# Performance work log

Hardware: AMD Instinct MI355X
Metric: run time of the kernel (lower is better)

The kernel has to match this reference:

```python
import jax, jax.numpy as jnp
import numpy as np

D = 1024
H = 8
DK = D // H
BS, NSEG, NSEN = 16, 64, 32


def _linear_params(key, d_in, d_out, scale=0.02):
    kw, kb = jax.random.split(key)
    w = jax.random.normal(kw, (d_out, d_in), dtype=jnp.float32) * scale
    b = jax.random.normal(kb, (d_out,), dtype=jnp.float32) * scale
    return w, b


def setup_inputs() -> dict:
    key = jax.random.key(0)
    ks = jax.random.split(key, 12)
    A = jax.random.normal(ks[0], (BS, NSEG, D), dtype=jnp.float32)
    V = jax.random.normal(ks[1], (BS, NSEG, D), dtype=jnp.float32)
    S = jax.random.normal(ks[2], (BS, NSEN, D), dtype=jnp.float32)
    wA, bA = _linear_params(ks[3], D, D)
    wV, bV = _linear_params(ks[4], D, D)
    wS, bS = _linear_params(ks[5], D, D)
    wq, bq = _linear_params(ks[6], D, D)
    wk, bk = _linear_params(ks[7], D, D)
    wv, bv = _linear_params(ks[8], D, D)
    w1, b1 = _linear_params(ks[9], D, D)
    w2, b2 = _linear_params(ks[10], D, D)
    return {"A": A, "V": V, "S": S,
            "wA": wA, "bA": bA, "wV": wV, "bV": bV, "wS": wS, "bS": bS,
            "wq": wq, "bq": bq, "wk": wk, "bk": bk, "wv": wv, "bv": bv,
            "w1": w1, "b1": b1, "w2": w2, "b2": b2}


def _lin(x, w, b):
    return x @ w.T + b


def reference(A, V, S, wA, bA, wV, bV, wS, bS, wq, bq, wk, bk, wv, bv, w1, b1, w2, b2):
    bs, num_seg, d_model = A.shape
    num_sen = S.shape[1]
    A = _lin(A, wA, bA)
    V = _lin(V, wV, bV)
    S = _lin(S, wS, bS)
    av = jnp.stack([A, V], axis=2)                       # (bs, num_seg, 2, d)
    q = _lin(S, wq, bq).reshape(bs, num_sen, H, DK)      # (b, s, h, dk)
    k = _lin(av, wk, bk).reshape(bs, num_seg, 2, H, DK)  # (b, g, a, h, dk)
    v = _lin(av, wv, bv).reshape(bs, num_seg, 2, H, DK)
    # attention over the size-2 A/V axis only
    attn = jnp.einsum('bshd,bgahd->bsgah', q, k) / np.sqrt(DK).astype(np.float32)
    attn = jax.nn.softmax(attn, axis=3)                  # softmax over a (A vs V)
    out = jnp.einsum('bsgah,bgahd->bsghd', attn, v)
    out = out.reshape(bs, num_sen, num_seg, d_model)
    # positionwise FF: Linear -> ReLU -> Linear (dropout p=0)
    out = _lin(jax.nn.relu(_lin(out, w1, b1)), w2, b2)
    return out
```

## Files before the change

kernel.cpp:

```cpp
#include <hip/hip_runtime.h>
#include <stdint.h>


#define D_MODEL 1024
#define N_HEAD  8
#define DK      128
#define BS      16
#define NSEG    64
#define NSEN    32

typedef __attribute__((ext_vector_type(8))) __bf16 bf16x8;
typedef __attribute__((ext_vector_type(8))) unsigned short u16x8;
typedef __attribute__((ext_vector_type(4))) float f32x4;

__device__ __forceinline__ float bf2f(unsigned short b) {
  union { unsigned int u; float f; } x; x.u = ((unsigned int)b) << 16; return x.f;
}
__device__ __forceinline__ unsigned short f2bf(float f) {
  union { float f; unsigned int u; } x; x.f = f;
  unsigned int u = x.u;
  unsigned int r = (u + 0x7fffu + ((u >> 16) & 1u)) >> 16;
  return (unsigned short)r;
}

__device__ __forceinline__ void g2l16(const void* g, void* l) {
  __builtin_amdgcn_global_load_lds(
      (const __attribute__((address_space(1))) void*)g,
      (__attribute__((address_space(3))) void*)l, 16, 0, 0);
}

struct CvtB { const float* s[11]; unsigned short* d[11]; int n4[11]; };
__global__ __launch_bounds__(256)
void cvtall_kernel(CvtB p) {
  const int z = blockIdx.y;
  const int i = blockIdx.x * 256 + threadIdx.x;
  if (i >= p.n4[z]) return;
  float4 v = reinterpret_cast<const float4*>(p.s[z])[i];
  ushort4 o;
  o.x = f2bf(v.x); o.y = f2bf(v.y); o.z = f2bf(v.z); o.w = f2bf(v.w);
  reinterpret_cast<ushort4*>(p.d[z])[i] = o;
}

struct GSeg { const unsigned short* A; const unsigned short* B;
              const float* bias; unsigned short* C; };
struct GBatch { GSeg s[3]; int end[3]; };

__global__ __launch_bounds__(256, 3)
void gemm128_bt(GBatch gb) {
  __shared__ __align__(16) unsigned short lds[3 * 8192];

  const int nwg = gridDim.x;
  const int sw = (blockIdx.x & 7) * (nwg >> 3) + (blockIdx.x >> 3);
  int sgi = 0, base = 0;
  if (sw >= gb.end[0]) { sgi = 1; base = gb.end[0]; }
  if (sw >= gb.end[1]) { sgi = 2; base = gb.end[1]; }
  const GSeg sg = gb.s[sgi];
  const int st = sw - base;
  const int m0 = (st >> 3) * 128, n0 = (st & 7) * 128;

  const int T = threadIdx.x;
  const int lane = T & 63, wave = T >> 6;
  const int wr = wave >> 1, wc = wave & 1;
  const int fr = lane & 15, kg = lane >> 4;

  char* ldsc = (char*)lds;

  const int srow = T >> 2;
  const int gsl = ((T & 3) ^ ((srow & 3) ^ ((srow >> 2) & 3))) * 8;
  const unsigned short* A0 = sg.A + (size_t)(m0 + srow) * 1024 + gsl;
  const unsigned short* A1 = sg.A + (size_t)(m0 + 64 + srow) * 1024 + gsl;
  const unsigned short* B0 = sg.B + (size_t)(n0 + srow) * 1024 + gsl;
  const unsigned short* B1 = sg.B + (size_t)(n0 + 64 + srow) * 1024 + gsl;

  auto stage = [&](int buf, int k0) {
    char* d = ldsc + buf * 16384;
    g2l16(A0 + k0, d + T * 16);
    g2l16(A1 + k0, d + 4096 + T * 16);
    g2l16(B0 + k0, d + 8192 + T * 16);
    g2l16(B1 + k0, d + 12288 + T * 16);
  };

  int raddr[4], baddr[4];
#pragma unroll
  for (int mi = 0; mi < 4; ++mi) {
    int ra = wr * 64 + mi * 16 + fr;
    raddr[mi] = ra * 64 + ((kg ^ ((ra & 3) ^ ((ra >> 2) & 3))) * 16);
  }
#pragma unroll
  for (int ni = 0; ni < 4; ++ni) {
    int rb = wc * 64 + ni * 16 + fr;
    baddr[ni] = 8192 + rb * 64 + ((kg ^ ((rb & 3) ^ ((rb >> 2) & 3))) * 16);
  }

  f32x4 acc[4][4] = {};
  u16x8 f0[8], f1[8];

#define G128_LOAD(DST, BUF)                                                    \
  {                                                                            \
    const char* bp_ = ldsc + (BUF) * 16384;                                    \
    _Pragma("unroll")                                                          \
    for (int mi = 0; mi < 4; ++mi)                                             \
      DST[mi] = *reinterpret_cast<const u16x8*>(bp_ + raddr[mi]);              \
    _Pragma("unroll")                                                          \
    for (int ni = 0; ni < 4; ++ni)                                             \
      DST[4 + ni] = *reinterpret_cast<const u16x8*>(bp_ + baddr[ni]);          \
  }

#define G128_MFMA(SRC)                                                         \
  {                                                                            \
    __builtin_amdgcn_s_setprio(1);                                             \
    _Pragma("unroll")                                                          \
    for (int ni = 0; ni < 4; ++ni)                                             \
      _Pragma("unroll")                                                        \
      for (int mi = 0; mi < 4; ++mi)                                           \
        acc[ni][mi] = __builtin_amdgcn_mfma_f32_16x16x32_bf16(                 \
            __builtin_bit_cast(bf16x8, SRC[4 + ni]),                           \
            __builtin_bit_cast(bf16x8, SRC[mi]), acc[ni][mi], 0, 0, 0);        \
    __builtin_amdgcn_s_setprio(0);                                             \
  }

#define G128_ITER(T_, CUR, NXT)                                                \
  {                                                                            \
    if ((T_) + 2 < NT) stage(((T_) + 2) % 3, ((T_) + 2) * 32);                 \
    if ((T_) + 1 < NT) {                                                       \
      if ((T_) + 2 < NT) asm volatile("s_waitcnt vmcnt(4)" ::: "memory");      \
      else               asm volatile("s_waitcnt vmcnt(0)" ::: "memory");      \
      __builtin_amdgcn_s_barrier();                                            \
      G128_LOAD(NXT, ((T_) + 1) % 3);                                          \
    }                                                                          \
    G128_MFMA(CUR);                                                            \
  }

  const int NT = 32;
  stage(0, 0);
  stage(1, 32);
  asm volatile("s_waitcnt vmcnt(4)" ::: "memory");
  __builtin_amdgcn_s_barrier();
  G128_LOAD(f0, 0);

  for (int it = 0; it < NT; it += 2) {
    G128_ITER(it,     f0, f1);
    G128_ITER(it + 1, f1, f0);
  }

#pragma unroll
  for (int ni = 0; ni < 4; ++ni) {
    const int gn0 = n0 + wc * 64 + ni * 16 + kg * 4;
    const float4 bv = *reinterpret_cast<const float4*>(&sg.bias[gn0]);
#pragma unroll
    for (int mi = 0; mi < 4; ++mi) {
      const int gm = m0 + wr * 64 + mi * 16 + fr;
      ushort4 o;
      o.x = f2bf(acc[ni][mi][0] + bv.x);
      o.y = f2bf(acc[ni][mi][1] + bv.y);
      o.z = f2bf(acc[ni][mi][2] + bv.z);
      o.w = f2bf(acc[ni][mi][3] + bv.w);
      *reinterpret_cast<ushort4*>(&sg.C[(size_t)gm * 1024 + gn0]) = o;
    }
  }
}

__global__ __launch_bounds__(512, 4)
void ff2_gemm(const unsigned short* __restrict__ A, const unsigned short* __restrict__ B,
              const float* __restrict__ bias, float* __restrict__ C,
              int M, int N, int K) {
  __shared__ __align__(16) unsigned short lds[2 * 12288];

  const int nwg = gridDim.x;
  const int sw = (blockIdx.x & 7) * (nwg >> 3) + (blockIdx.x >> 3);
  const int m0 = (sw >> 3) * 256, n0 = (sw & 7) * 128;

  const int T = threadIdx.x;
  const int lane = T & 63, wave = T >> 6;
  const int wr = wave >> 1, wc = wave & 1;
  const int fr = lane & 15, kg = lane >> 4;
  const int NT = K >> 5;

  char* ldsc = (char*)lds;

  const int srow = T >> 2;
  const int gsl = ((T & 3) ^ ((srow & 3) ^ ((srow >> 2) & 3))) * 8;
  const unsigned short* A0 = A + (size_t)(m0 + srow) * K + gsl;
  const unsigned short* A1 = A + (size_t)(m0 + 128 + srow) * K + gsl;
  const unsigned short* B0 = B + (size_t)(n0 + srow) * K + gsl;

  auto stage = [&](int buf, int t) {
    const int kb = t * 32;
    char* dst = ldsc + buf * 24576 + T * 16;
    g2l16(A0 + kb, dst);
    g2l16(A1 + kb, dst + 8192);
    g2l16(B0 + kb, dst + 16384);
  };

  int raddr[4], baddr[4];
#pragma unroll
  for (int mi = 0; mi < 4; ++mi) {
    int lr = wr * 64 + mi * 16 + fr;
    raddr[mi] = lr * 64 + ((kg ^ ((lr & 3) ^ ((lr >> 2) & 3))) * 16);
  }
#pragma unroll
  for (int ni = 0; ni < 4; ++ni) {
    int lr = wc * 64 + ni * 16 + fr;
    baddr[ni] = 16384 + lr * 64 + ((kg ^ ((lr & 3) ^ ((lr >> 2) & 3))) * 16);
  }

  f32x4 acc[4][4] = {};

  stage(0, 0);
  asm volatile("s_waitcnt vmcnt(0)" ::: "memory");
  __builtin_amdgcn_s_barrier();

  for (int t = 0; t < NT; ++t) {
    const int buf = t & 1;
    if (t + 1 < NT) stage(buf ^ 1, t + 1);

    const char* base = ldsc + buf * 24576;
    u16x8 af[4], bf[4];
#pragma unroll
    for (int mi = 0; mi < 4; ++mi)
      af[mi] = *reinterpret_cast<const u16x8*>(base + raddr[mi]);
#pragma unroll
    for (int ni = 0; ni < 4; ++ni)
      bf[ni] = *reinterpret_cast<const u16x8*>(base + baddr[ni]);

    __builtin_amdgcn_s_setprio(1);
#pragma unroll
    for (int ni = 0; ni < 4; ++ni)
#pragma unroll
      for (int mi = 0; mi < 4; ++mi)
        acc[ni][mi] = __builtin_amdgcn_mfma_f32_16x16x32_bf16(
            __builtin_bit_cast(bf16x8, bf[ni]), __builtin_bit_cast(bf16x8, af[mi]),
            acc[ni][mi], 0, 0, 0);
    __builtin_amdgcn_s_setprio(0);

    asm volatile("s_waitcnt vmcnt(0)" ::: "memory");
    __builtin_amdgcn_s_barrier();
  }

#pragma unroll
  for (int ni = 0; ni < 4; ++ni) {
    const int gn0 = n0 + wc * 64 + ni * 16 + kg * 4;
    const float4 bv = *reinterpret_cast<const float4*>(&bias[gn0]);
#pragma unroll
    for (int mi = 0; mi < 4; ++mi) {
      const int gm = m0 + wr * 64 + mi * 16 + fr;
      float4 o;
      o.x = acc[ni][mi][0] + bv.x;
      o.y = acc[ni][mi][1] + bv.y;
      o.z = acc[ni][mi][2] + bv.z;
      o.w = acc[ni][mi][3] + bv.w;
      *reinterpret_cast<float4*>(&C[(size_t)gm * N + gn0]) = o;
    }
  }
}

__global__ __launch_bounds__(256)
void uav_gemm(const unsigned short* __restrict__ vAV, const unsigned short* __restrict__ w1,
              unsigned short* __restrict__ UAV) {
  __shared__ __align__(16) unsigned short lA[2][128 * 32];
  __shared__ __align__(16) unsigned short lB[2][128 * 32];

  const int zb = blockIdx.z;
  const int tensor = zb >> 3, h = zb & 7;
  const unsigned short* Ab = vAV + (size_t)tensor * (1024 * 1024) + h * 128;
  const unsigned short* Bb = w1 + h * 128;
  unsigned short* Cb = UAV + (size_t)tensor * (1024 * 8192) + h * 1024;

  const int t = threadIdx.x;
  const int m0 = blockIdx.y * 128, n0 = blockIdx.x * 128;
  const int lane = t & 63, wv = t >> 6;
  const int wrow = (wv >> 1) * 64, wcol = (wv & 1) * 64;
  const int fr = lane & 15, kg = lane >> 4;

  f32x4 acc[4][4] = {};

  const int r  = t >> 2;
  const int c8 = (t & 3) * 8;
  const unsigned short* ga = Ab + (size_t)(m0 + r) * 1024 + c8;
  const unsigned short* gb = Bb + (size_t)(n0 + r) * 1024 + c8;

  auto stage = [&](int buf, int k0) {
    g2l16(ga + k0,             &lA[buf][t * 8]);
    g2l16(ga + k0 + 64 * 1024, &lA[buf][2048 + t * 8]);
    g2l16(gb + k0,             &lB[buf][t * 8]);
    g2l16(gb + k0 + 64 * 1024, &lB[buf][2048 + t * 8]);
  };

  stage(0, 0);
  asm volatile("s_waitcnt vmcnt(0)" ::: "memory");
  __syncthreads();

  for (int k0 = 0; k0 < 128; k0 += 32) {
    const int buf = (k0 >> 5) & 1;
    if (k0 + 32 < 128) stage(buf ^ 1, k0 + 32);

    u16x8 af[4], bg_[4];
#pragma unroll
    for (int mi = 0; mi < 4; ++mi)
      af[mi] = *reinterpret_cast<const u16x8*>(&lA[buf][(wrow + mi * 16 + fr) * 32 + kg * 8]);
#pragma unroll
    for (int ni = 0; ni < 4; ++ni)
      bg_[ni] = *reinterpret_cast<const u16x8*>(&lB[buf][(wcol + ni * 16 + fr) * 32 + kg * 8]);
#pragma unroll
    for (int ni = 0; ni < 4; ++ni)
#pragma unroll
      for (int mi = 0; mi < 4; ++mi)
        acc[ni][mi] = __builtin_amdgcn_mfma_f32_16x16x32_bf16(
            __builtin_bit_cast(bf16x8, bg_[ni]), __builtin_bit_cast(bf16x8, af[mi]),
            acc[ni][mi], 0, 0, 0);

    asm volatile("s_waitcnt vmcnt(0)" ::: "memory");
    __syncthreads();
  }

#pragma unroll
  for (int ni = 0; ni < 4; ++ni) {
    const int gn0 = n0 + wcol + ni * 16 + kg * 4;
#pragma unroll
    for (int mi = 0; mi < 4; ++mi) {
      const int gm = m0 + wrow + mi * 16 + fr;
      ushort4 o;
      o.x = f2bf(acc[ni][mi][0]);
      o.y = f2bf(acc[ni][mi][1]);
      o.z = f2bf(acc[ni][mi][2]);
      o.w = f2bf(acc[ni][mi][3]);
      *reinterpret_cast<ushort4*>(&Cb[(size_t)gm * 8192 + gn0]) = o;
    }
  }
}

__global__ __launch_bounds__(256)
void score_hid_kernel(const unsigned short* __restrict__ q,
                      const unsigned short* __restrict__ kAV,
                      const unsigned short* __restrict__ UAV,
                      const float* __restrict__ b1,
                      unsigned short* __restrict__ hid) {
  const int bg = blockIdx.x;
  const int b = bg >> 6, g = bg & 63;
  __shared__ float sk[2][D_MODEL];
  __shared__ float pAl[NSEN][N_HEAD];
  const size_t rowA = (size_t)bg * D_MODEL;
  const size_t rowV = rowA + (size_t)BS * NSEG * D_MODEL;
  for (int i = threadIdx.x; i < D_MODEL; i += 256) {
    sk[0][i] = bf2f(kAV[rowA + i]);
    sk[1][i] = bf2f(kAV[rowV + i]);
  }
  __syncthreads();

  const int h = threadIdx.x >> 5;
  const int l = threadIdx.x & 31;
  const float scale = 0.08838834764831845f;

  for (int s = 0; s < NSEN; ++s) {
    const unsigned short* pq = q + ((size_t)(b * NSEN + s)) * D_MODEL + h * DK;
    float la = 0.f, lv = 0.f;
#pragma unroll
    for (int e = 0; e < 4; ++e) {
      int d = l + e * 32;
      float qv = bf2f(pq[d]);
      la += qv * sk[0][h * DK + d];
      lv += qv * sk[1][h * DK + d];
    }
#pragma unroll
    for (int off = 16; off; off >>= 1) {
      la += __shfl_xor(la, off, 32);
      lv += __shfl_xor(lv, off, 32);
    }
    if (l == 0) pAl[s][h] = 1.f / (1.f + __expf((lv - la) * scale));
  }
  __syncthreads();

  const int tn = (threadIdx.x & 127) * 8;
  const int sb = (threadIdx.x >> 7) * 16;
  const unsigned short* ua = UAV + (size_t)bg * 8192 + tn;
  const unsigned short* uv = ua + (size_t)1024 * 8192;

  float dU[N_HEAD][8];
  float base[8];
#pragma unroll
  for (int j = 0; j < 8; ++j) base[j] = b1[tn + j];
#pragma unroll
  for (int hh = 0; hh < N_HEAD; ++hh) {
    u16x8 a8 = *reinterpret_cast<const u16x8*>(ua + hh * 1024);
    u16x8 v8 = *reinterpret_cast<const u16x8*>(uv + hh * 1024);
#pragma unroll
    for (int j = 0; j < 8; ++j) {
      float va = bf2f(a8[j]), vv = bf2f(v8[j]);
      dU[hh][j] = va - vv; base[j] += vv;
    }
  }

  for (int s = sb; s < sb + 16; ++s) {
    float val[8];
#pragma unroll
    for (int j = 0; j < 8; ++j) val[j] = base[j];
#pragma unroll
    for (int hh = 0; hh < N_HEAD; ++hh) {
      const float p = pAl[s][hh];
#pragma unroll
      for (int j = 0; j < 8; ++j) val[j] = fmaf(p, dU[hh][j], val[j]);
    }
    u16x8 o;
#pragma unroll
    for (int j = 0; j < 8; ++j) o[j] = f2bf(val[j] > 0.f ? val[j] : 0.f);
    size_t orow = ((size_t)(b * NSEN + s) * NSEG + g) * D_MODEL + tn;
    *reinterpret_cast<u16x8*>(hid + orow) = o;
  }
}

extern "C" void kernel_launch(void* const* d_in, const int* in_sizes, int n_in,
                              void* d_out, int out_size, void* d_ws, size_t ws_size,
                              hipStream_t stream) {
  const float* A  = (const float*)d_in[0];
  const float* V  = (const float*)d_in[1];
  const float* S  = (const float*)d_in[2];
  const float* wA = (const float*)d_in[3];  const float* bA = (const float*)d_in[4];
  const float* wV = (const float*)d_in[5];  const float* bV = (const float*)d_in[6];
  const float* wS = (const float*)d_in[7];  const float* bS = (const float*)d_in[8];
  const float* wq = (const float*)d_in[9];  const float* bq = (const float*)d_in[10];
  const float* wk = (const float*)d_in[11]; const float* bk = (const float*)d_in[12];
  const float* wv = (const float*)d_in[13]; const float* bv = (const float*)d_in[14];
  const float* w1 = (const float*)d_in[15]; const float* b1 = (const float*)d_in[16];
  const float* w2 = (const float*)d_in[17]; const float* b2 = (const float*)d_in[18];

  const int nAV = BS * NSEG * D_MODEL;
  const int nS  = BS * NSEN * D_MODEL;
  const int nW  = D_MODEL * D_MODEL;
  const int nCT = BS * NSEN * NSEG * D_MODEL;
  const int nU  = 2 * 1024 * 8 * 1024;

  char* ws = (char*)d_ws;
  size_t off = 0;
  auto carve = [&](size_t elems) {
    unsigned short* p = (unsigned short*)(ws + off);
    off += elems * sizeof(unsigned short);
    return p;
  };
  unsigned short* bwA = carve(nW);
  unsigned short* bwV = carve(nW);
  unsigned short* bwS = carve(nW);
  unsigned short* bwq = carve(nW);
  unsigned short* bwk = carve(nW);
  unsigned short* bwv = carve(nW);
  unsigned short* bw1 = carve(nW);
  unsigned short* bw2 = carve(nW);
  unsigned short* xA  = carve(nAV);
  unsigned short* xV  = carve(nAV);
  unsigned short* xS  = carve(nS);
  unsigned short* A1V1 = carve(2 * nAV);
  unsigned short* S1  = carve(nS);
  unsigned short* qb  = carve(nS);
  unsigned short* kAV = carve(2 * nAV);
  unsigned short* vAV = carve(2 * nAV);
  unsigned short* UAV = carve(nU);
  unsigned short* hid = carve(nCT);
  (void)ws_size; (void)n_in; (void)in_sizes; (void)out_size;

  CvtB cv;
  cv.s[0] = wA; cv.d[0] = bwA; cv.n4[0] = nW / 4;
  cv.s[1] = wV; cv.d[1] = bwV; cv.n4[1] = nW / 4;
  cv.s[2] = wS; cv.d[2] = bwS; cv.n4[2] = nW / 4;
  cv.s[3] = wq; cv.d[3] = bwq; cv.n4[3] = nW / 4;
  cv.s[4] = wk; cv.d[4] = bwk; cv.n4[4] = nW / 4;
  cv.s[5] = wv; cv.d[5] = bwv; cv.n4[5] = nW / 4;
  cv.s[6] = w1; cv.d[6] = bw1; cv.n4[6] = nW / 4;
  cv.s[7] = w2; cv.d[7] = bw2; cv.n4[7] = nW / 4;
  cv.s[8] = A;  cv.d[8] = xA;  cv.n4[8] = nAV / 4;
  cv.s[9] = V;  cv.d[9] = xV;  cv.n4[9] = nAV / 4;
  cv.s[10] = S; cv.d[10] = xS; cv.n4[10] = nS / 4;
  cvtall_kernel<<<dim3(1024, 11), dim3(256), 0, stream>>>(cv);

  GBatch pj;
  pj.s[0] = {xA, bwA, bA, A1V1};        pj.end[0] = 64;
  pj.s[1] = {xV, bwV, bV, A1V1 + nAV};  pj.end[1] = 128;
  pj.s[2] = {xS, bwS, bS, S1};          pj.end[2] = 160;
  gemm128_bt<<<dim3(160), 256, 0, stream>>>(pj);

  GBatch qkv;
  qkv.s[0] = {S1,   bwq, bq, qb};   qkv.end[0] = 32;
  qkv.s[1] = {A1V1, bwk, bk, kAV};  qkv.end[1] = 160;
  qkv.s[2] = {A1V1, bwv, bv, vAV};  qkv.end[2] = 288;
  gemm128_bt<<<dim3(288), 256, 0, stream>>>(qkv);

  uav_gemm<<<dim3(8, 8, 16), dim3(256), 0, stream>>>(vAV, bw1, UAV);

  score_hid_kernel<<<dim3(BS * NSEG), dim3(256), 0, stream>>>(qb, kAV, UAV, b1, hid);

  ff2_gemm<<<dim3(1024), 512, 0, stream>>>(hid, bw2, b2, (float*)d_out,
                                           32768, 1024, 1024);
}
```

Baseline: 209.4 us.

## Enlarge ff2 GEMM tile to 256x256 with 4 waves of 128x128

The final FF2 GEMM moves from 256x128 tiles with 8 waves (64x64 per wave) to 256x256 tiles with 4 waves, each computing 128x128 via an 8x8 MFMA grid. The aim is higher arithmetic intensity per LDS read and fewer global loads of A and B per output, with half as many workgroups. In exchange each thread holds 256 accumulator floats, which risks register pressure or spills, and fewer waves per CU reduce latency hiding. A 512-workgroup grid may also balance unevenly across the CUs.

```diff
diff --git a/kernel.cpp b/kernel.cpp
--- a/kernel.cpp
+++ b/kernel.cpp
@@ -160,15 +160,15 @@
   }
 }
 
-__global__ __launch_bounds__(512, 4)
+__global__ __launch_bounds__(256, 2)
 void ff2_gemm(const unsigned short* __restrict__ A, const unsigned short* __restrict__ B,
               const float* __restrict__ bias, float* __restrict__ C,
               int M, int N, int K) {
-  __shared__ __align__(16) unsigned short lds[2 * 12288];
+  __shared__ __align__(16) unsigned short lds[2 * 16384];
 
   const int nwg = gridDim.x;
   const int sw = (blockIdx.x & 7) * (nwg >> 3) + (blockIdx.x >> 3);
-  const int m0 = (sw >> 3) * 256, n0 = (sw & 7) * 128;
+  const int m0 = (sw >> 2) * 256, n0 = (sw & 3) * 256;
 
   const int T = threadIdx.x;
   const int lane = T & 63, wave = T >> 6;
@@ -180,31 +180,41 @@
 
   const int srow = T >> 2;
   const int gsl = ((T & 3) ^ ((srow & 3) ^ ((srow >> 2) & 3))) * 8;
-  const unsigned short* A0 = A + (size_t)(m0 + srow) * K + gsl;
-  const unsigned short* A1 = A + (size_t)(m0 + 128 + srow) * K + gsl;
-  const unsigned short* B0 = B + (size_t)(n0 + srow) * K + gsl;
+  const unsigned short* Ar0 = A + (size_t)(m0 + srow) * K + gsl;
+  const unsigned short* Ar1 = A + (size_t)(m0 + 64 + srow) * K + gsl;
+  const unsigned short* Ar2 = A + (size_t)(m0 + 128 + srow) * K + gsl;
+  const unsigned short* Ar3 = A + (size_t)(m0 + 192 + srow) * K + gsl;
+  const unsigned short* Br0 = B + (size_t)(n0 + srow) * K + gsl;
+  const unsigned short* Br1 = B + (size_t)(n0 + 64 + srow) * K + gsl;
+  const unsigned short* Br2 = B + (size_t)(n0 + 128 + srow) * K + gsl;
+  const unsigned short* Br3 = B + (size_t)(n0 + 192 + srow) * K + gsl;
 
   auto stage = [&](int buf, int t) {
     const int kb = t * 32;
-    char* dst = ldsc + buf * 24576 + T * 16;
-    g2l16(A0 + kb, dst);
-    g2l16(A1 + kb, dst + 8192);
-    g2l16(B0 + kb, dst + 16384);
+    char* d = ldsc + buf * 32768 + T * 16;
+    g2l16(Ar0 + kb, d);
+    g2l16(Ar1 + kb, d + 4096);
+    g2l16(Ar2 + kb, d + 8192);
+    g2l16(Ar3 + kb, d + 12288);
+    g2l16(Br0 + kb, d + 16384);
+    g2l16(Br1 + kb, d + 20480);
+    g2l16(Br2 + kb, d + 24576);
+    g2l16(Br3 + kb, d + 28672);
   };
 
-  int raddr[4], baddr[4];
-#pragma unroll
-  for (int mi = 0; mi < 4; ++mi) {
-    int lr = wr * 64 + mi * 16 + fr;
-    raddr[mi] = lr * 64 + ((kg ^ ((lr & 3) ^ ((lr >> 2) & 3))) * 16);
-  }
-#pragma unroll
-  for (int ni = 0; ni < 4; ++ni) {
-    int lr = wc * 64 + ni * 16 + fr;
-    baddr[ni] = 16384 + lr * 64 + ((kg ^ ((lr & 3) ^ ((lr >> 2) & 3))) * 16);
-  }
-
-  f32x4 acc[4][4] = {};
+  int raddr[8], baddr[8];
+#pragma unroll
+  for (int mi = 0; mi < 8; ++mi) {
+    int ra = wr * 128 + mi * 16 + fr;
+    raddr[mi] = ra * 64 + ((kg ^ ((ra & 3) ^ ((ra >> 2) & 3))) * 16);
+  }
+#pragma unroll
+  for (int ni = 0; ni < 8; ++ni) {
+    int rb = wc * 128 + ni * 16 + fr;
+    baddr[ni] = 16384 + rb * 64 + ((kg ^ ((rb & 3) ^ ((rb >> 2) & 3))) * 16);
+  }
+
+  f32x4 acc[8][8] = {};
 
   stage(0, 0);
   asm volatile("s_waitcnt vmcnt(0)" ::: "memory");
@@ -214,20 +224,20 @@
     const int buf = t & 1;
     if (t + 1 < NT) stage(buf ^ 1, t + 1);
 
-    const char* base = ldsc + buf * 24576;
-    u16x8 af[4], bf[4];
-#pragma unroll
-    for (int mi = 0; mi < 4; ++mi)
+    const char* base = ldsc + buf * 32768;
+    u16x8 af[8], bf[8];
+#pragma unroll
+    for (int mi = 0; mi < 8; ++mi)
       af[mi] = *reinterpret_cast<const u16x8*>(base + raddr[mi]);
 #pragma unroll
-    for (int ni = 0; ni < 4; ++ni)
+    for (int ni = 0; ni < 8; ++ni)
       bf[ni] = *reinterpret_cast<const u16x8*>(base + baddr[ni]);
 
     __builtin_amdgcn_s_setprio(1);
 #pragma unroll
-    for (int ni = 0; ni < 4; ++ni)
-#pragma unroll
-      for (int mi = 0; mi < 4; ++mi)
+    for (int ni = 0; ni < 8; ++ni)
+#pragma unroll
+      for (int mi = 0; mi < 8; ++mi)
         acc[ni][mi] = __builtin_amdgcn_mfma_f32_16x16x32_bf16(
             __builtin_bit_cast(bf16x8, bf[ni]), __builtin_bit_cast(bf16x8, af[mi]),
             acc[ni][mi], 0, 0, 0);
@@ -238,12 +248,12 @@
   }
 
 #pragma unroll
-  for (int ni = 0; ni < 4; ++ni) {
-    const int gn0 = n0 + wc * 64 + ni * 16 + kg * 4;
+  for (int ni = 0; ni < 8; ++ni) {
+    const int gn0 = n0 + wc * 128 + ni * 16 + kg * 4;
     const float4 bv = *reinterpret_cast<const float4*>(&bias[gn0]);
 #pragma unroll
-    for (int mi = 0; mi < 4; ++mi) {
-      const int gm = m0 + wr * 64 + mi * 16 + fr;
+    for (int mi = 0; mi < 8; ++mi) {
+      const int gm = m0 + wr * 128 + mi * 16 + fr;
       float4 o;
       o.x = acc[ni][mi][0] + bv.x;
       o.y = acc[ni][mi][1] + bv.y;
@@ -486,6 +496,6 @@
 
   score_hid_kernel<<<dim3(BS * NSEG), dim3(256), 0, stream>>>(qb, kAV, UAV, b1, hid);
 
-  ff2_gemm<<<dim3(1024), 512, 0, stream>>>(hid, bw2, b2, (float*)d_out,
-                                           32768, 1024, 1024);
-}
+  ff2_gemm<<<dim3(512), 256, 0, stream>>>(hid, bw2, b2, (float*)d_out,
+                                          32768, 1024, 1024);
+}
```

Result: slower. 590.9 us (+182.2%).
